# Kernel tuning notes

Measured on AMD Instinct MI355X. Metric: run time of the kernel, lower is better.

Reference implementation:

```python
import jax, jax.numpy as jnp
import numpy as np


def setup_inputs() -> dict:
    key = jax.random.key(0)
    ks = jax.random.split(key, 7)
    B, C, H, W = 8, 256, 64, 64
    Cp = C // 8
    sc = 1.0 / np.sqrt(C)
    return {
        "x": jax.random.normal(ks[0], (B, C, H, W), dtype=jnp.float32),
        "Wq": jax.random.normal(ks[1], (Cp, C), dtype=jnp.float32) * sc,
        "bq": jnp.zeros((Cp,), dtype=jnp.float32),
        "Wk": jax.random.normal(ks[2], (Cp, C), dtype=jnp.float32) * sc,
        "bk": jnp.zeros((Cp,), dtype=jnp.float32),
        "Wv": jax.random.normal(ks[3], (C, C), dtype=jnp.float32) * sc,
        "bv": jnp.zeros((C,), dtype=jnp.float32),
        "gamma": jnp.float32(0.5),
    }


def reference(x, Wq, bq, Wk, bk, Wv, bv, gamma):
    B, C, H, W = x.shape
    xf = x.reshape(B, C, H * W)                         # (B, C, N)
    # 1x1 Conv1d == per-position linear over channels
    q = jnp.einsum('dc,bcn->bnd', Wq, xf) + bq          # (B, N, Cp)
    k = jnp.einsum('dc,bcn->bdn', Wk, xf) + bk[:, None] # (B, Cp, N)
    v = jnp.einsum('dc,bcn->bdn', Wv, xf) + bv[:, None] # (B, C, N)
    scores = jnp.einsum('bnd,bdm->bnm', q, k)           # (B, N, N)
    attn = jax.nn.softmax(scores, axis=-1)              # (B, N, N)
    # o = v @ attn^T : o[:, :, n] = sum_m attn[n, m] * v[:, :, m]
    o = jnp.einsum('bcm,bnm->bcn', v, attn)             # (B, C, N)
    o = o.reshape(B, C, H, W)
    return gamma * o + x
```

## Files before the change

### kernel.cpp

```cpp
#include <hip/hip_runtime.h>
#include <hip/hip_bf16.h>


constexpr int C  = 256;
constexpr int CP = 32;
constexpr int NPOS = 4096;
constexpr int NB = 8;
constexpr int MT = 64;
constexpr int NT = NPOS / MT;

typedef __attribute__((ext_vector_type(4))) float  f32x4;
typedef __attribute__((ext_vector_type(4))) short  bf16x4;
typedef __attribute__((ext_vector_type(8))) short  bf16x8;

__device__ __forceinline__ void bar_lds() {
    asm volatile("s_waitcnt lgkmcnt(0)\n\ts_barrier" ::: "memory");
}
__device__ __forceinline__ void wait_vm1() {
    asm volatile("s_waitcnt vmcnt(1)" ::: "memory");
}
__device__ __forceinline__ void wait_vm5() {
    asm volatile("s_waitcnt vmcnt(5)" ::: "memory");
}
__device__ __forceinline__ void gl_lds16(const void* gsrc, void* ldst) {
    typedef const __attribute__((address_space(1))) void* gp_t;
    typedef __attribute__((address_space(3))) void* lp_t;
    __builtin_amdgcn_global_load_lds((gp_t)gsrc, (lp_t)ldst, 16, 0, 0);
}
__device__ __forceinline__ short f2bf(float f) {
    __hip_bfloat16 h = __float2bfloat16(f);
    return __builtin_bit_cast(short, h);
}
__device__ __forceinline__ f32x4 mfma16(bf16x8 a, bf16x8 b, f32x4 c) {
    return __builtin_amdgcn_mfma_f32_16x16x32_bf16(a, b, c, 0, 0, 0);
}

__global__ __launch_bounds__(256) void wprep_kernel(
    const float* __restrict__ Wq, const float* __restrict__ bq,
    const float* __restrict__ Wk, const float* __restrict__ bk,
    const float* __restrict__ Wv, const float* __restrict__ bv,
    __hip_bfloat16* __restrict__ wh, __hip_bfloat16* __restrict__ wl,
    float* __restrict__ bcat)
{
    const int r = blockIdx.x, c = threadIdx.x;
    float w;
    if (r < 32)      w = Wq[r * 256 + c];
    else if (r < 64) w = Wk[(r - 32) * 256 + c];
    else             w = Wv[(r - 64) * 256 + c];
    __hip_bfloat16 h = __float2bfloat16(w);
    wh[r * 256 + c] = h;
    wl[r * 256 + c] = __float2bfloat16(w - __bfloat162float(h));
    if (c == 0)
        bcat[r] = (r < 32) ? bq[r] : (r < 64) ? bk[r - 32] : bv[r - 64];
}

__global__ __launch_bounds__(256) void xtrans_kernel(
    const float* __restrict__ x, __hip_bfloat16* __restrict__ xT)
{
    __shared__ float xl[64][65];
    const int tid = threadIdx.x;
    const int b   = blockIdx.x >> 8;
    const int rem = blockIdx.x & 255;
    const int c0  = (rem >> 6) << 6;
    const int n0  = (rem & 63) << 6;

    const float* xb = x + ((size_t)b * C + c0) * NPOS + n0;
    #pragma unroll
    for (int k = 0; k < 4; ++k) {
        const int idx = tid + k * 256;
        const int c = idx >> 4, j4 = idx & 15;
        float4 gg = *reinterpret_cast<const float4*>(xb + (size_t)c * NPOS + j4 * 4);
        xl[c][j4 * 4 + 0] = gg.x; xl[c][j4 * 4 + 1] = gg.y;
        xl[c][j4 * 4 + 2] = gg.z; xl[c][j4 * 4 + 3] = gg.w;
    }
    __syncthreads();

    const int nl = tid >> 2, cseg = tid & 3;
    bf16x8 o0, o1;
    #pragma unroll
    for (int j = 0; j < 8; ++j) {
        o0[j] = f2bf(xl[cseg * 16 + j][nl]);
        o1[j] = f2bf(xl[cseg * 16 + 8 + j][nl]);
    }
    __hip_bfloat16* dst = xT + ((size_t)b * NPOS + n0 + nl) * C + c0 + cseg * 16;
    *reinterpret_cast<bf16x8*>(dst)     = o0;
    *reinterpret_cast<bf16x8*>(dst + 8) = o1;
}

__global__ __launch_bounds__(512)
__attribute__((amdgpu_waves_per_eu(4)))
void qkv_mfma_kernel(
    const __hip_bfloat16* __restrict__ xT,
    const __hip_bfloat16* __restrict__ wh, const __hip_bfloat16* __restrict__ wl,
    const float* __restrict__ bcat,
    __hip_bfloat16* __restrict__ qh, __hip_bfloat16* __restrict__ ql,
    __hip_bfloat16* __restrict__ kh, __hip_bfloat16* __restrict__ kl,
    __hip_bfloat16* __restrict__ vT)
{
    __shared__ __align__(16) __hip_bfloat16 xlds[16384];
    __shared__ __align__(16) __hip_bfloat16 wlds[3][4096];

    const int tid = threadIdx.x;
    const int b  = blockIdx.x & 7;
    const int n0 = (blockIdx.x >> 3) << 6;
    const int l  = tid & 63;
    const int g  = tid >> 6;
    const int G  = l >> 4;
    const int li = l & 15;
    const int cs = g >> 1, ns0 = (g & 1) * 2;

    #pragma unroll
    for (int j = 0; j < 4; ++j)
        gl_lds16(xT + ((size_t)b * NPOS + n0 + l) * C + (j * 8 + g) * 8,
                 xlds + (j * 512 + g * 64) * 8);

    auto stageW = [&](int t, int d) {
        const int ct = t >> 3, ks = t & 7;
        const __hip_bfloat16* src = (g < 4) ? wh : wl;
        const int gg = g & 3;
        gl_lds16(src + (size_t)(ct * 64 + l) * 256 + ks * 32 + gg * 8,
                 &wlds[d][((g >= 4) ? 2048 : 0) + gg * 512]);
    };
    stageW(0, 0);
    stageW(1, 1);

    f32x4 acc0 = (f32x4){0.f, 0.f, 0.f, 0.f};
    f32x4 acc1 = (f32x4){0.f, 0.f, 0.f, 0.f};
    const float gammaless = 0.f; (void)gammaless;

    for (int t = 0; t < 40; ++t) {
        wait_vm1();
        bar_lds();
        if (t + 2 < 40) stageW(t + 2, (t + 2) % 3);

        const int ks = t & 7;
        const __hip_bfloat16* wb = wlds[t % 3];
        bf16x8 whf = *reinterpret_cast<const bf16x8*>(wb + (G * 64 + cs * 16 + li) * 8);
        bf16x8 wlf = *reinterpret_cast<const bf16x8*>(wb + 2048 + (G * 64 + cs * 16 + li) * 8);
        bf16x8 xf0 = *reinterpret_cast<const bf16x8*>(
            xlds + (ks * 256 + G * 64 + ns0 * 16 + li) * 8);
        bf16x8 xf1 = *reinterpret_cast<const bf16x8*>(
            xlds + (ks * 256 + G * 64 + (ns0 + 1) * 16 + li) * 8);
        acc0 = mfma16(whf, xf0, acc0);
        acc0 = mfma16(wlf, xf0, acc0);
        acc1 = mfma16(whf, xf1, acc1);
        acc1 = mfma16(wlf, xf1, acc1);

        if (ks == 7) {
            const int ct = t >> 3;
            const int cb = ct * 64 + cs * 16 + G * 4;
            const float4 b4 = *reinterpret_cast<const float4*>(bcat + cb);
            const float bb[4] = {b4.x, b4.y, b4.z, b4.w};
            #pragma unroll
            for (int j = 0; j < 2; ++j) {
                const f32x4 a = j ? acc1 : acc0;
                const int n_abs = n0 + (ns0 + j) * 16 + li;
                if (ct == 0) {
                    __hip_bfloat16* hb = (cs < 2) ? qh : kh;
                    __hip_bfloat16* lb = (cs < 2) ? ql : kl;
                    const int cq = (cs < 2) ? cb : cb - 32;
                    const size_t base = ((size_t)b * NPOS + n_abs) * CP + cq;
                    #pragma unroll
                    for (int r = 0; r < 4; ++r) {
                        const float val = a[r] + bb[r];
                        __hip_bfloat16 h = __float2bfloat16(val);
                        hb[base + r] = h;
                        lb[base + r] = __float2bfloat16(val - __bfloat162float(h));
                    }
                } else {
                    const int cv = cb - 64;
                    #pragma unroll
                    for (int r = 0; r < 4; ++r)
                        vT[((size_t)b * C + cv + r) * NPOS + n_abs] =
                            __float2bfloat16(a[r] + bb[r]);
                }
            }
            acc0 = (f32x4){0.f, 0.f, 0.f, 0.f};
            acc1 = (f32x4){0.f, 0.f, 0.f, 0.f};
        }
    }
}

__global__ __launch_bounds__(512)
__attribute__((amdgpu_waves_per_eu(4)))
void attn_kernel(
    const __hip_bfloat16* __restrict__ qh, const __hip_bfloat16* __restrict__ ql,
    const __hip_bfloat16* __restrict__ kh, const __hip_bfloat16* __restrict__ kl,
    const __hip_bfloat16* __restrict__ vT, const float* __restrict__ x,
    const float* __restrict__ gamma_p, float* __restrict__ out)
{
    __shared__ __align__(16) __hip_bfloat16 k_lds[2][2][2048];
    __shared__ __align__(16) __hip_bfloat16 v_lds[8][2][1024];
    __shared__ __align__(16) __hip_bfloat16 p_lds[4096];
    __shared__ float pmx[2][64];
    __shared__ float psm[2][64];
    __shared__ float scale_lds[64];
    __shared__ float lsums[64];

    const int tid = threadIdx.x;
    const int b  = blockIdx.x & 7;
    const int qt = blockIdx.x >> 3;
    const int l  = tid & 63;
    const int g  = tid >> 6;
    const int G  = l >> 4;
    const int li = l & 15;
    const int nj = g & 3, gr = g >> 2;
    const int mi0 = gr * 2;
    const int sn = nj * 16 + li;

    const __hip_bfloat16* khb = kh + (size_t)b * NPOS * CP;
    const __hip_bfloat16* klb = kl + (size_t)b * NPOS * CP;
    const __hip_bfloat16* vTb = vT + (size_t)b * C * NPOS;

    bf16x8 qhf, qlf;
    {
        const size_t qoff = ((size_t)b * NPOS + qt * 64 + nj * 16 + li) * CP + G * 8;
        qhf = *reinterpret_cast<const bf16x8*>(qh + qoff);
        qlf = *reinterpret_cast<const bf16x8*>(ql + qoff);
    }

    f32x4 acc[4][2];
    #pragma unroll
    for (int nt = 0; nt < 4; ++nt)
        #pragma unroll
        for (int ct = 0; ct < 2; ++ct) acc[nt][ct] = (f32x4){0.f, 0.f, 0.f, 0.f};
    float mx_reg = -1e30f, lsum_reg = 0.f;
    f32x4 sacc0, sacc1;

    auto stageK = [&](int tt, int bufd) {
        const __hip_bfloat16* ks = (gr == 0) ? khb : klb;
        gl_lds16(ks + (size_t)tt * MT * CP + l * CP + nj * 8,
                 &k_lds[bufd][gr][nj * 512]);
    };
    auto stageV = [&](int tt) {
        #pragma unroll
        for (int ct = 0; ct < 2; ++ct)
            #pragma unroll
            for (int s = 0; s < 2; ++s)
                gl_lds16(vTb + (size_t)(g * 32 + ct * 16 + li) * NPOS
                             + tt * MT + s * 32 + G * 8,
                         &v_lds[g][ct][s * 512]);
    };
    auto qk_phase = [&](int bufq) {
        const int kfo = (G * 64 + mi0 * 16 + li) * 8;
        bf16x8 kh0 = *reinterpret_cast<const bf16x8*>(&k_lds[bufq][0][kfo]);
        bf16x8 kl0 = *reinterpret_cast<const bf16x8*>(&k_lds[bufq][1][kfo]);
        bf16x8 kh1 = *reinterpret_cast<const bf16x8*>(&k_lds[bufq][0][kfo + 128]);
        bf16x8 kl1 = *reinterpret_cast<const bf16x8*>(&k_lds[bufq][1][kfo + 128]);
        f32x4 s0 = (f32x4){0.f, 0.f, 0.f, 0.f};
        s0 = mfma16(kh0, qhf, s0); s0 = mfma16(kh0, qlf, s0); s0 = mfma16(kl0, qhf, s0);
        f32x4 s1 = (f32x4){0.f, 0.f, 0.f, 0.f};
        s1 = mfma16(kh1, qhf, s1); s1 = mfma16(kh1, qlf, s1); s1 = mfma16(kl1, qhf, s1);
        sacc0 = s0; sacc1 = s1;
        float m4 = fmaxf(fmaxf(fmaxf(s0[0], s0[1]), fmaxf(s0[2], s0[3])),
                         fmaxf(fmaxf(s1[0], s1[1]), fmaxf(s1[2], s1[3])));
        m4 = fmaxf(m4, __shfl_xor(m4, 16));
        m4 = fmaxf(m4, __shfl_xor(m4, 32));
        if (G == 0) pmx[gr][sn] = m4;
    };

    stageK(0, 0);
    stageK(1, 1);
    stageV(0);
    wait_vm5();
    bar_lds();
    qk_phase(0);
    bar_lds();

    for (int t = 0; t < NT; ++t) {
        const int buf = t & 1;

        stageK((t + 2) & (NT - 1), buf);
        const float tm = fmaxf(pmx[0][sn], pmx[1][sn]);
        const float nm = fmaxf(mx_reg, tm);
        const float scale_own = __expf(mx_reg - nm);
        mx_reg = nm;
        float p0[4], p1[4];
        #pragma unroll
        for (int r = 0; r < 4; ++r) {
            p0[r] = __expf(sacc0[r] - nm);
            p1[r] = __expf(sacc1[r] - nm);
        }
        float ps = ((p0[0] + p0[1]) + (p0[2] + p0[3]))
                 + ((p1[0] + p1[1]) + (p1[2] + p1[3]));
        ps += __shfl_xor(ps, 16);
        ps += __shfl_xor(ps, 32);
        if (G == 0) psm[gr][sn] = ps;
        {
            const int ms0 = mi0 * 4 + G;
            bf16x4 w0 = { f2bf(p0[0]), f2bf(p0[1]), f2bf(p0[2]), f2bf(p0[3]) };
            *reinterpret_cast<bf16x4*>(p_lds + ms0 * 256 + ((sn ^ ms0) * 4)) = w0;
            const int ms1 = ms0 + 4;
            bf16x4 w1 = { f2bf(p1[0]), f2bf(p1[1]), f2bf(p1[2]), f2bf(p1[3]) };
            *reinterpret_cast<bf16x4*>(p_lds + ms1 * 256 + ((sn ^ ms1) * 4)) = w1;
        }
        if (g < 4 && G == 0) scale_lds[sn] = scale_own;
        wait_vm5();
        bar_lds();

        wait_vm1();
        lsum_reg = lsum_reg * scale_own + psm[0][sn] + psm[1][sn];
        float scl[4];
        #pragma unroll
        for (int nt = 0; nt < 4; ++nt) scl[nt] = scale_lds[nt * 16 + li];
        #pragma unroll
        for (int nt = 0; nt < 4; ++nt) {
            acc[nt][0] *= scl[nt];
            acc[nt][1] *= scl[nt];
        }
        #pragma unroll
        for (int s = 0; s < 2; ++s) {
            bf16x8 af0 = *reinterpret_cast<const bf16x8*>(
                &v_lds[g][0][s * 512 + G * 128 + li * 8]);
            bf16x8 af1 = *reinterpret_cast<const bf16x8*>(
                &v_lds[g][1][s * 512 + G * 128 + li * 8]);
            bf16x8 bfr[4];
            #pragma unroll
            for (int nt = 0; nt < 4; ++nt) {
                const int n = nt * 16 + li;
                const int ma = s * 8 + 2 * G, mb = ma + 1;
                bf16x4 blo = *reinterpret_cast<const bf16x4*>(
                    p_lds + ma * 256 + ((n ^ ma) * 4));
                bf16x4 bhi = *reinterpret_cast<const bf16x4*>(
                    p_lds + mb * 256 + ((n ^ mb) * 4));
                bfr[nt] = __builtin_shufflevector(blo, bhi, 0,1,2,3,4,5,6,7);
            }
            #pragma unroll
            for (int nt = 0; nt < 4; ++nt) {
                acc[nt][0] = mfma16(af0, bfr[nt], acc[nt][0]);
                acc[nt][1] = mfma16(af1, bfr[nt], acc[nt][1]);
            }
        }
        if (t + 1 < NT) qk_phase(buf ^ 1);
        __builtin_amdgcn_sched_barrier(0);
        stageV((t + 1) & (NT - 1));
        bar_lds();
    }

    if (g < 4 && G == 0) lsums[sn] = lsum_reg;
    bar_lds();
    const float gamma = *gamma_p;
    const float* xb = x   + (size_t)b * C * NPOS;
    float*       ob = out + (size_t)b * C * NPOS;

    #pragma unroll
    for (int nt = 0; nt < 4; ++nt) {
        const float inv = 1.0f / lsums[nt * 16 + li];
        const int n = qt * 64 + nt * 16 + li;
        #pragma unroll
        for (int ct = 0; ct < 2; ++ct) {
            const int c0 = g * 32 + ct * 16 + G * 4;
            #pragma unroll
            for (int r = 0; r < 4; ++r) {
                const size_t idx = (size_t)(c0 + r) * NPOS + n;
                ob[idx] = gamma * acc[nt][ct][r] * inv + xb[idx];
            }
        }
    }
}

extern "C" void kernel_launch(void* const* d_in, const int* in_sizes, int n_in,
                              void* d_out, int out_size, void* d_ws, size_t ws_size,
                              hipStream_t stream) {
    const float* x  = (const float*)d_in[0];
    const float* Wq = (const float*)d_in[1];
    const float* bq = (const float*)d_in[2];
    const float* Wk = (const float*)d_in[3];
    const float* bk = (const float*)d_in[4];
    const float* Wv = (const float*)d_in[5];
    const float* bv = (const float*)d_in[6];
    const float* gamma = (const float*)d_in[7];
    float* out = (float*)d_out;

    const size_t qk_n = (size_t)NB * NPOS * CP;
    const size_t v_n  = (size_t)NB * C * NPOS;
    __hip_bfloat16* qhb = (__hip_bfloat16*)d_ws;
    __hip_bfloat16* qlb = qhb + qk_n;
    __hip_bfloat16* khb = qlb + qk_n;
    __hip_bfloat16* klb = khb + qk_n;
    __hip_bfloat16* vT  = klb + qk_n;
    __hip_bfloat16* xT  = vT + v_n;
    __hip_bfloat16* wh  = xT + v_n;
    __hip_bfloat16* wl  = wh + 320 * 256;
    float*          bcat = (float*)(wl + 320 * 256);

    xtrans_kernel<<<NB * 4 * 64, 256, 0, stream>>>(x, xT);
    wprep_kernel<<<320, 256, 0, stream>>>(Wq, bq, Wk, bk, Wv, bv, wh, wl, bcat);
    qkv_mfma_kernel<<<NB * (NPOS / 64), 512, 0, stream>>>(xT, wh, wl, bcat,
                                                          qhb, qlb, khb, klb, vT);
    attn_kernel<<<NB * (NPOS / 64), 512, 0, stream>>>(qhb, qlb, khb, klb, vT,
                                                      x, gamma, out);
}
```

Baseline: 191.9 us.

## Load V fragments directly to registers, use exp2 with log2e-scaled Q, add setprio

V tiles are no longer staged through LDS with global_load_lds. Each wave now loads its own V fragments straight from global memory into registers at the top of each iteration, removing the v_lds buffer and its synchronization. The softmax exponentials switch to exp2, with LOG2E folded into Q at projection time, and s_setprio raises wave priority around the MFMA region. The risk is that global-load latency is exposed within the same iteration, since loads are issued only one phase before use, and the vmcnt waits were reworked accordingly.

```diff
diff --git a/kernel.cpp b/kernel.cpp
--- a/kernel.cpp
+++ b/kernel.cpp
@@ -8,6 +8,7 @@
 constexpr int NB = 8;
 constexpr int MT = 64;
 constexpr int NT = NPOS / MT;
+constexpr float LOG2E = 1.44269504088896340736f;
 
 typedef __attribute__((ext_vector_type(4))) float  f32x4;
 typedef __attribute__((ext_vector_type(4))) short  bf16x4;
@@ -30,6 +31,9 @@
 __device__ __forceinline__ short f2bf(float f) {
     __hip_bfloat16 h = __float2bfloat16(f);
     return __builtin_bit_cast(short, h);
+}
+__device__ __forceinline__ float ex2(float f) {
+    return __builtin_amdgcn_exp2f(f);
 }
 __device__ __forceinline__ f32x4 mfma16(bf16x8 a, bf16x8 b, f32x4 c) {
     return __builtin_amdgcn_mfma_f32_16x16x32_bf16(a, b, c, 0, 0, 0);
@@ -126,7 +130,6 @@
 
     f32x4 acc0 = (f32x4){0.f, 0.f, 0.f, 0.f};
     f32x4 acc1 = (f32x4){0.f, 0.f, 0.f, 0.f};
-    const float gammaless = 0.f; (void)gammaless;
 
     for (int t = 0; t < 40; ++t) {
         wait_vm1();
@@ -158,11 +161,12 @@
                 if (ct == 0) {
                     __hip_bfloat16* hb = (cs < 2) ? qh : kh;
                     __hip_bfloat16* lb = (cs < 2) ? ql : kl;
+                    const float qsc = (cs < 2) ? LOG2E : 1.0f;
                     const int cq = (cs < 2) ? cb : cb - 32;
                     const size_t base = ((size_t)b * NPOS + n_abs) * CP + cq;
                     #pragma unroll
                     for (int r = 0; r < 4; ++r) {
-                        const float val = a[r] + bb[r];
+                        const float val = (a[r] + bb[r]) * qsc;
                         __hip_bfloat16 h = __float2bfloat16(val);
                         hb[base + r] = h;
                         lb[base + r] = __float2bfloat16(val - __bfloat162float(h));
@@ -190,7 +194,6 @@
     const float* __restrict__ gamma_p, float* __restrict__ out)
 {
     __shared__ __align__(16) __hip_bfloat16 k_lds[2][2][2048];
-    __shared__ __align__(16) __hip_bfloat16 v_lds[8][2][1024];
     __shared__ __align__(16) __hip_bfloat16 p_lds[4096];
     __shared__ float pmx[2][64];
     __shared__ float psm[2][64];
@@ -219,6 +222,9 @@
         qlf = *reinterpret_cast<const bf16x8*>(ql + qoff);
     }
 
+    const __hip_bfloat16* vp0 = vTb + (size_t)(g * 32 + li) * NPOS + G * 8;
+    const __hip_bfloat16* vp1 = vTb + (size_t)(g * 32 + 16 + li) * NPOS + G * 8;
+
     f32x4 acc[4][2];
     #pragma unroll
     for (int nt = 0; nt < 4; ++nt)
@@ -231,15 +237,6 @@
         const __hip_bfloat16* ks = (gr == 0) ? khb : klb;
         gl_lds16(ks + (size_t)tt * MT * CP + l * CP + nj * 8,
                  &k_lds[bufd][gr][nj * 512]);
-    };
-    auto stageV = [&](int tt) {
-        #pragma unroll
-        for (int ct = 0; ct < 2; ++ct)
-            #pragma unroll
-            for (int s = 0; s < 2; ++s)
-                gl_lds16(vTb + (size_t)(g * 32 + ct * 16 + li) * NPOS
-                             + tt * MT + s * 32 + G * 8,
-                         &v_lds[g][ct][s * 512]);
     };
     auto qk_phase = [&](int bufq) {
         const int kfo = (G * 64 + mi0 * 16 + li) * 8;
@@ -261,8 +258,7 @@
 
     stageK(0, 0);
     stageK(1, 1);
-    stageV(0);
-    wait_vm5();
+    wait_vm1();
     bar_lds();
     qk_phase(0);
     bar_lds();
@@ -270,16 +266,22 @@
     for (int t = 0; t < NT; ++t) {
         const int buf = t & 1;
 
+        bf16x8 vf00 = *reinterpret_cast<const bf16x8*>(vp0);
+        bf16x8 vf01 = *reinterpret_cast<const bf16x8*>(vp0 + 32);
+        bf16x8 vf10 = *reinterpret_cast<const bf16x8*>(vp1);
+        bf16x8 vf11 = *reinterpret_cast<const bf16x8*>(vp1 + 32);
+        __builtin_amdgcn_sched_barrier(0);
         stageK((t + 2) & (NT - 1), buf);
+
         const float tm = fmaxf(pmx[0][sn], pmx[1][sn]);
         const float nm = fmaxf(mx_reg, tm);
-        const float scale_own = __expf(mx_reg - nm);
+        const float scale_own = ex2(mx_reg - nm);
         mx_reg = nm;
         float p0[4], p1[4];
         #pragma unroll
         for (int r = 0; r < 4; ++r) {
-            p0[r] = __expf(sacc0[r] - nm);
-            p1[r] = __expf(sacc1[r] - nm);
+            p0[r] = ex2(sacc0[r] - nm);
+            p1[r] = ex2(sacc1[r] - nm);
         }
         float ps = ((p0[0] + p0[1]) + (p0[2] + p0[3]))
                  + ((p1[0] + p1[1]) + (p1[2] + p1[3]));
@@ -298,7 +300,6 @@
         wait_vm5();
         bar_lds();
 
-        wait_vm1();
         lsum_reg = lsum_reg * scale_own + psm[0][sn] + psm[1][sn];
         float scl[4];
         #pragma unroll
@@ -308,12 +309,11 @@
             acc[nt][0] *= scl[nt];
             acc[nt][1] *= scl[nt];
         }
+        __builtin_amdgcn_s_setprio(1);
         #pragma unroll
         for (int s = 0; s < 2; ++s) {
-            bf16x8 af0 = *reinterpret_cast<const bf16x8*>(
-                &v_lds[g][0][s * 512 + G * 128 + li * 8]);
-            bf16x8 af1 = *reinterpret_cast<const bf16x8*>(
-                &v_lds[g][1][s * 512 + G * 128 + li * 8]);
+            const bf16x8 af0 = s ? vf01 : vf00;
+            const bf16x8 af1 = s ? vf11 : vf10;
             bf16x8 bfr[4];
             #pragma unroll
             for (int nt = 0; nt < 4; ++nt) {
@@ -332,9 +332,10 @@
             }
         }
         if (t + 1 < NT) qk_phase(buf ^ 1);
-        __builtin_amdgcn_sched_barrier(0);
-        stageV((t + 1) & (NT - 1));
+        __builtin_amdgcn_s_setprio(0);
         bar_lds();
+        vp0 += MT;
+        vp1 += MT;
     }
 
     if (g < 4 && G == 0) lsums[sn] = lsum_reg;
```

Measured after the change: 185.6 us. 1.03x faster.
